# Kernel optimization log

Hardware: AMD Instinct MI355X
Metric: run time of the kernel (lower is better)

## Reference

```python
import jax, jax.numpy as jnp
import numpy as np


def setup_inputs() -> dict:
    key = jax.random.key(0)
    k1, k2 = jax.random.split(key)
    B, HW, C, M, P = 8, 4096, 1024, 32, 512
    feature_map = jax.random.normal(k1, (B, HW, C), dtype=jnp.float32)
    # normalized (y, x) coords in [0,1], as produced by mask.nonzero()/[H,W]
    point_coords = jax.random.uniform(k2, (B, M, P, 2), dtype=jnp.float32)
    return {"feature_map": feature_map, "point_coords": point_coords}


def reference(feature_map, point_coords):
    # feature_map: [B, H*W, C]; point_coords: [B, M, P, 2] as (y_norm, x_norm).
    B, HW, C = feature_map.shape
    h = w = int(np.sqrt(HW))
    # torch flips coords to (x, y); grid_sample(align_corners=True) maps
    # grid g = 2*coord-1 to pixel coord*(size-1).
    y = point_coords[..., 0] * (h - 1)  # [B, M, P]
    x = point_coords[..., 1] * (w - 1)
    x0f = jnp.floor(x)
    y0f = jnp.floor(y)
    wx = (x - x0f)[..., None]  # [B, M, P, 1]
    wy = (y - y0f)[..., None]
    ix0 = jnp.clip(x0f.astype(jnp.int32), 0, w - 1)
    ix1 = jnp.clip(ix0 + 1, 0, w - 1)
    iy0 = jnp.clip(y0f.astype(jnp.int32), 0, h - 1)
    iy1 = jnp.clip(iy0 + 1, 0, h - 1)

    def gather(iy, ix):
        idx = (iy * w + ix).reshape(B, -1)  # [B, M*P]
        g = jnp.take_along_axis(feature_map, idx[:, :, None], axis=1)  # [B, M*P, C]
        return g.reshape(B, iy.shape[1], iy.shape[2], C)

    f00 = gather(iy0, ix0)
    f01 = gather(iy0, ix1)
    f10 = gather(iy1, ix0)
    f11 = gather(iy1, ix1)
    # bilinear interpolation -> [B, M, P, C]
    sampled = (f00 * (1 - wx) * (1 - wy) + f01 * wx * (1 - wy)
               + f10 * (1 - wx) * wy + f11 * wx * wy)
    # AdaptiveAvgPool1d(1) over points, then transpose -> [B, M, 1, C]
    region_feat = jnp.mean(sampled, axis=2, keepdims=True)
    return region_feat
```

## Files before the change

kernel.cpp:

```cpp
#include <hip/hip_runtime.h>
#include <stdint.h>


#define NB 8
#define NM 32
#define NP 512
#define NC 1024
#define NH 64
#define NHW 4096

#define NKC  32
#define ROWS (NHW / NKC)
#define KT   8
#define NT   (ROWS / KT)
#define NCT  4
#define CTW  256

__device__ __forceinline__ void async16(const void* g, void* l) {
    __builtin_amdgcn_global_load_lds(
        (const __attribute__((address_space(1))) unsigned int*)g,
        (__attribute__((address_space(3))) unsigned int*)l,
        16, 0, 0);
}

__global__ __launch_bounds__(256) void scatter_w(
    const float* __restrict__ pc, float* __restrict__ W)
{
    int idx = blockIdx.x * 256 + threadIdx.x;
    int bm  = idx >> 9;
    int m   = bm & (NM - 1);
    int b   = bm >> 5;

    float2 c = ((const float2*)pc)[idx];
    float y = c.x * 63.0f;
    float x = c.y * 63.0f;
    float x0f = floorf(x), y0f = floorf(y);
    float wx = x - x0f, wy = y - y0f;
    int ix0 = min(max((int)x0f, 0), 63);
    int ix1 = min(ix0 + 1, 63);
    int iy0 = min(max((int)y0f, 0), 63);
    int iy1 = min(iy0 + 1, 63);
    float wx1 = 1.0f - wx, wy1 = 1.0f - wy;
    const float s = 1.0f / (float)NP;

    float* Wb = W + (size_t)b * (NHW * NM) + m;
    atomicAdd(Wb + ((iy0 * NH + ix0) * NM), wx1 * wy1 * s);
    atomicAdd(Wb + ((iy0 * NH + ix1) * NM), wx  * wy1 * s);
    atomicAdd(Wb + ((iy1 * NH + ix0) * NM), wx1 * wy  * s);
    atomicAdd(Wb + ((iy1 * NH + ix1) * NM), wx  * wy  * s);
}

__global__ __launch_bounds__(256) void wgemm(
    const float* __restrict__ W, const float* __restrict__ F,
    float* __restrict__ P)
{
    __shared__ float4 sF[2][KT * CTW / 4];
    __shared__ float4 sWt[ROWS * NM / 4];

    const int kc   = blockIdx.x;
    const int ct   = blockIdx.y;
    const int b    = blockIdx.z;
    const int tid  = threadIdx.x;
    const int wav  = tid >> 6;
    const int lane = tid & 63;
    const int hw0  = kc * ROWS;
    const int wq   = wav * 2;
    const int c0   = ct * CTW + lane * 4;
    const int lane16 = lane * 16;

    const char* Wg = (const char*)(W + ((size_t)b * NHW + hw0) * NM);
    const char* Fg = (const char*)(F + ((size_t)b * NHW + hw0) * NC + ct * CTW);

    {
        char* lds = (char*)sWt;
#pragma unroll
        for (int i = 0; i < 4; ++i) {
            int j = wav * 4 + i;
            async16(Wg + j * 1024 + lane16, lds + j * 1024 + lane16);
        }
    }
    auto stage_f = [&](int t, int buf) {
        char* lds = (char*)sF[buf];
#pragma unroll
        for (int i = 0; i < 2; ++i) {
            int j = wav * 2 + i;
            async16(Fg + (size_t)(t * KT + j) * (NC * 4) + lane16,
                    lds + j * 1024 + lane16);
        }
    };

    stage_f(0, 0);
    __syncthreads();

    float4 acc[8];
#pragma unroll
    for (int m = 0; m < 8; ++m) acc[m] = make_float4(0.f, 0.f, 0.f, 0.f);

    for (int t = 0; t < NT; ++t) {
        if (t + 1 < NT) stage_f(t + 1, (t + 1) & 1);
        const float4* fb = sF[t & 1];
        const float4* wr = sWt + (size_t)(t * KT) * (NM / 4);
#pragma unroll
        for (int r = 0; r < KT; ++r) {
            float4 f  = fb[r * 64 + lane];
            float4 wa = wr[r * 8 + wq];
            float4 wb = wr[r * 8 + wq + 1];
            float wv[8] = {wa.x, wa.y, wa.z, wa.w, wb.x, wb.y, wb.z, wb.w};
#pragma unroll
            for (int m = 0; m < 8; ++m) {
                acc[m].x = fmaf(wv[m], f.x, acc[m].x);
                acc[m].y = fmaf(wv[m], f.y, acc[m].y);
                acc[m].z = fmaf(wv[m], f.z, acc[m].z);
                acc[m].w = fmaf(wv[m], f.w, acc[m].w);
            }
        }
        __syncthreads();
    }

    float* pb = P + (((size_t)kc * NB + b) * NM + wav * 8) * NC + c0;
#pragma unroll
    for (int m = 0; m < 8; ++m)
        *(float4*)(pb + (size_t)m * NC) = acc[m];
}

__global__ __launch_bounds__(256) void reduce_p(
    const float* __restrict__ P, float* __restrict__ out)
{
    const int idx = blockIdx.x * 256 + threadIdx.x;
    const float4* p4 = (const float4*)P;
    const int stride = NB * NM * NC / 4;
    float4 s = make_float4(0.f, 0.f, 0.f, 0.f);
#pragma unroll
    for (int kc = 0; kc < NKC; ++kc) {
        float4 v = p4[(size_t)kc * stride + idx];
        s.x += v.x; s.y += v.y; s.z += v.z; s.w += v.w;
    }
    ((float4*)out)[idx] = s;
}

__global__ __launch_bounds__(256) void region_pool_direct(
    const float* __restrict__ fm, const float* __restrict__ pc,
    float* __restrict__ out)
{
    __shared__ int4   sIdx[NP];
    __shared__ float4 sWv[NP];
    const int bid = blockIdx.x;
    const int b   = bid >> 5;
    const int tid = threadIdx.x;
    const float2* pc2 = (const float2*)(pc + (size_t)bid * NP * 2);
    for (int p = tid; p < NP; p += 256) {
        float2 c = pc2[p];
        float y = c.x * 63.0f, x = c.y * 63.0f;
        float x0f = floorf(x), y0f = floorf(y);
        float wx = x - x0f, wy = y - y0f;
        int ix0 = min(max((int)x0f, 0), 63);
        int ix1 = min(ix0 + 1, 63);
        int iy0 = min(max((int)y0f, 0), 63);
        int iy1 = min(iy0 + 1, 63);
        sIdx[p] = make_int4((iy0 * NH + ix0) << 10, (iy0 * NH + ix1) << 10,
                            (iy1 * NH + ix0) << 10, (iy1 * NH + ix1) << 10);
        float wx1 = 1.0f - wx, wy1 = 1.0f - wy;
        sWv[p] = make_float4(wx1 * wy1, wx * wy1, wx1 * wy, wx * wy);
    }
    __syncthreads();
    const float* Fb = fm + (size_t)b * (NHW * NC) + tid * 4;
    float4 acc = make_float4(0.f, 0.f, 0.f, 0.f);
#pragma unroll 4
    for (int p = 0; p < NP; ++p) {
        int4 off = sIdx[p]; float4 w = sWv[p];
        float4 f00 = *(const float4*)(Fb + off.x);
        float4 f01 = *(const float4*)(Fb + off.y);
        float4 f10 = *(const float4*)(Fb + off.z);
        float4 f11 = *(const float4*)(Fb + off.w);
        acc.x = fmaf(w.x, f00.x, fmaf(w.y, f01.x, fmaf(w.z, f10.x, fmaf(w.w, f11.x, acc.x))));
        acc.y = fmaf(w.x, f00.y, fmaf(w.y, f01.y, fmaf(w.z, f10.y, fmaf(w.w, f11.y, acc.y))));
        acc.z = fmaf(w.x, f00.z, fmaf(w.y, f01.z, fmaf(w.z, f10.z, fmaf(w.w, f11.z, acc.z))));
        acc.w = fmaf(w.x, f00.w, fmaf(w.y, f01.w, fmaf(w.z, f10.w, fmaf(w.w, f11.w, acc.w))));
    }
    const float inv = 1.0f / (float)NP;
    ((float4*)(out + (size_t)bid * NC))[tid] =
        make_float4(acc.x * inv, acc.y * inv, acc.z * inv, acc.w * inv);
}

extern "C" void kernel_launch(void* const* d_in, const int* in_sizes, int n_in,
                              void* d_out, int out_size, void* d_ws, size_t ws_size,
                              hipStream_t stream) {
    const float* fm = (const float*)d_in[0];
    const float* pc = (const float*)d_in[1];
    float* out = (float*)d_out;

    const size_t wbytes = (size_t)NB * NHW * NM * sizeof(float);
    const size_t pbytes = (size_t)NKC * NB * NM * NC * sizeof(float);
    if (ws_size >= wbytes + pbytes) {
        float* W = (float*)d_ws;
        float* P = (float*)((char*)d_ws + wbytes);
        hipMemsetAsync(W, 0, wbytes, stream);
        scatter_w<<<(NB * NM * NP) / 256, 256, 0, stream>>>(pc, W);
        dim3 grid(NKC, NCT, NB);
        wgemm<<<grid, 256, 0, stream>>>(W, fm, P);
        reduce_p<<<(NB * NM * NC / 4) / 256, 256, 0, stream>>>(P, out);
    } else {
        region_pool_direct<<<NB * NM, 256, 0, stream>>>(fm, pc, out);
    }
}
```

Measured before the change: 238.3 us.

## Double K-split count, read W via scalar loads, dual-accumulator reduction

Raises the number of K-chunks in the weighted GEMM from 32 to 64, doubling the grid to fill more CUs on the 4096-row reduction. The W tile is no longer staged through LDS. Each wave now reads its 8 weight columns directly from global memory, using a wave-uniform pointer so the compiler can emit scalar loads, which frees LDS and removes that prologue load. The reduce kernel uses two accumulators to cover the doubled partial count, at the cost of twice as much partial-sum traffic to write and read.

```diff
diff --git a/kernel.cpp b/kernel.cpp
--- a/kernel.cpp
+++ b/kernel.cpp
@@ -9,7 +9,7 @@
 #define NH 64
 #define NHW 4096
 
-#define NKC  32
+#define NKC  64
 #define ROWS (NHW / NKC)
 #define KT   8
 #define NT   (ROWS / KT)
@@ -55,30 +55,20 @@
     float* __restrict__ P)
 {
     __shared__ float4 sF[2][KT * CTW / 4];
-    __shared__ float4 sWt[ROWS * NM / 4];
 
     const int kc   = blockIdx.x;
     const int ct   = blockIdx.y;
     const int b    = blockIdx.z;
     const int tid  = threadIdx.x;
-    const int wav  = tid >> 6;
+    const int wav  = __builtin_amdgcn_readfirstlane(tid >> 6);
     const int lane = tid & 63;
     const int hw0  = kc * ROWS;
-    const int wq   = wav * 2;
     const int c0   = ct * CTW + lane * 4;
     const int lane16 = lane * 16;
 
-    const char* Wg = (const char*)(W + ((size_t)b * NHW + hw0) * NM);
+    const float* __restrict__ Wu = W + ((size_t)b * NHW + hw0) * NM + wav * 8;
     const char* Fg = (const char*)(F + ((size_t)b * NHW + hw0) * NC + ct * CTW);
 
-    {
-        char* lds = (char*)sWt;
-#pragma unroll
-        for (int i = 0; i < 4; ++i) {
-            int j = wav * 4 + i;
-            async16(Wg + j * 1024 + lane16, lds + j * 1024 + lane16);
-        }
-    }
     auto stage_f = [&](int t, int buf) {
         char* lds = (char*)sF[buf];
 #pragma unroll
@@ -99,19 +89,17 @@
     for (int t = 0; t < NT; ++t) {
         if (t + 1 < NT) stage_f(t + 1, (t + 1) & 1);
         const float4* fb = sF[t & 1];
-        const float4* wr = sWt + (size_t)(t * KT) * (NM / 4);
 #pragma unroll
         for (int r = 0; r < KT; ++r) {
-            float4 f  = fb[r * 64 + lane];
-            float4 wa = wr[r * 8 + wq];
-            float4 wb = wr[r * 8 + wq + 1];
-            float wv[8] = {wa.x, wa.y, wa.z, wa.w, wb.x, wb.y, wb.z, wb.w};
+            float4 f = fb[r * 64 + lane];
+            const float* __restrict__ wr = Wu + (size_t)(t * KT + r) * NM;
 #pragma unroll
             for (int m = 0; m < 8; ++m) {
-                acc[m].x = fmaf(wv[m], f.x, acc[m].x);
-                acc[m].y = fmaf(wv[m], f.y, acc[m].y);
-                acc[m].z = fmaf(wv[m], f.z, acc[m].z);
-                acc[m].w = fmaf(wv[m], f.w, acc[m].w);
+                float w = wr[m];
+                acc[m].x = fmaf(w, f.x, acc[m].x);
+                acc[m].y = fmaf(w, f.y, acc[m].y);
+                acc[m].z = fmaf(w, f.z, acc[m].z);
+                acc[m].w = fmaf(w, f.w, acc[m].w);
             }
         }
         __syncthreads();
@@ -129,13 +117,17 @@
     const int idx = blockIdx.x * 256 + threadIdx.x;
     const float4* p4 = (const float4*)P;
     const int stride = NB * NM * NC / 4;
-    float4 s = make_float4(0.f, 0.f, 0.f, 0.f);
-#pragma unroll
-    for (int kc = 0; kc < NKC; ++kc) {
-        float4 v = p4[(size_t)kc * stride + idx];
-        s.x += v.x; s.y += v.y; s.z += v.z; s.w += v.w;
+    float4 s0 = make_float4(0.f, 0.f, 0.f, 0.f);
+    float4 s1 = make_float4(0.f, 0.f, 0.f, 0.f);
+#pragma unroll 8
+    for (int kc = 0; kc < NKC; kc += 2) {
+        float4 a = p4[(size_t)kc * stride + idx];
+        float4 c = p4[(size_t)(kc + 1) * stride + idx];
+        s0.x += a.x; s0.y += a.y; s0.z += a.z; s0.w += a.w;
+        s1.x += c.x; s1.y += c.y; s1.z += c.z; s1.w += c.w;
     }
-    ((float4*)out)[idx] = s;
+    ((float4*)out)[idx] = make_float4(s0.x + s1.x, s0.y + s1.y,
+                                      s0.z + s1.z, s0.w + s1.w);
 }
 
 __global__ __launch_bounds__(256) void region_pool_direct(
```

Result: no change. 239.2 us (+0.4%).
